# Performance work log

Measured on AMD Instinct MI355X. Metric: run time of the kernel, lower is better.

## Reference

```python
import jax, jax.numpy as jnp
import numpy as np
from jax import lax

B, T, D_IN, D_CB, K_CB, H_MID = 32, 512, 1024, 256, 8192, 512

def setup_inputs() -> dict:
    key = jax.random.key(0)
    ks = jax.random.split(key, 12)
    s = 0.02
    return {
        "x": jax.random.normal(ks[0], (B, T, D_IN), jnp.float32),
        "w1": jax.random.normal(ks[1], (H_MID, D_IN), jnp.float32) * s,
        "b1": jnp.zeros((H_MID,), jnp.float32),
        "w2": jax.random.normal(ks[2], (D_CB, H_MID), jnp.float32) * s,
        "b2": jnp.zeros((D_CB,), jnp.float32),
        "conv_w": jax.random.normal(ks[3], (D_CB, D_CB, 3), jnp.float32) * s,
        "conv_b": jnp.zeros((D_CB,), jnp.float32),
        "codebook": jax.random.uniform(ks[4], (K_CB, D_CB), jnp.float32, -1.0 / K_CB, 1.0 / K_CB),
        "gru_wih": jax.random.normal(ks[5], (3 * D_CB, D_CB), jnp.float32) * s,
        "gru_whh": jax.random.normal(ks[6], (3 * D_CB, D_CB), jnp.float32) * s,
        "gru_bih": jnp.zeros((3 * D_CB,), jnp.float32),
        "gru_bhh": jnp.zeros((3 * D_CB,), jnp.float32),
    }

def _forward(x, w1, b1, w2, b2, conv_w, conv_b, codebook, gru_wih, gru_whh, gru_bih, gru_bhh):
    # feature_processor (dropout is identity at eval): [B,T,D_IN] -> [B,T,D_CB]
    h = jax.nn.relu(jnp.einsum('btd,hd->bth', x, w1) + b1)
    h = jax.nn.relu(jnp.einsum('bth,ch->btc', h, w2) + b2)
    # temporal conv1d, kernel 3, pad 1 (T > 1 here)
    f = jnp.transpose(h, (0, 2, 1))  # NCT
    f = lax.conv_general_dilated(f, conv_w, (1,), 'SAME', dimension_numbers=('NCH', 'OIH', 'NCH'))
    f = f + conv_b[None, :, None]
    features = jnp.transpose(f, (0, 2, 1))  # [B,T,D_CB]
    # quantize: squared-Euclidean nearest codebook entry (same argmin as cdist)
    flat = features.reshape(-1, features.shape[-1])  # [B*T, D_CB]
    d2 = (jnp.sum(flat * flat, axis=1, keepdims=True)
          - 2.0 * (flat @ codebook.T)
          + jnp.sum(codebook * codebook, axis=1))  # [B*T, K]
    idx = jnp.argmin(d2, axis=-1)
    quantized = codebook[idx].reshape(features.shape)  # [B,T,D_CB]
    token_indices = idx.reshape(features.shape[0], features.shape[1])
    commitment_loss = jnp.mean((features - lax.stop_gradient(quantized)) ** 2)
    codebook_loss = jnp.mean((quantized - lax.stop_gradient(features)) ** 2)
    # context predictor: 1-layer GRU over quantized[:, :-1]
    q_in = quantized[:, :-1]  # [B,T-1,D_CB]
    xproj = jnp.einsum('btd,hd->bth', q_in, gru_wih) + gru_bih  # [B,T-1,3H]
    Hd = quantized.shape[-1]
    def step(hprev, xt):
        gh = hprev @ gru_whh.T + gru_bhh  # [B,3H]
        xr, xz, xn = xt[:, :Hd], xt[:, Hd:2 * Hd], xt[:, 2 * Hd:]
        hr, hz, hn = gh[:, :Hd], gh[:, Hd:2 * Hd], gh[:, 2 * Hd:]
        r = jax.nn.sigmoid(xr + hr)
        z = jax.nn.sigmoid(xz + hz)
        n = jnp.tanh(xn + r * hn)
        hnew = (1.0 - z) * n + z * hprev
        return hnew, hnew
    h0 = jnp.zeros((q_in.shape[0], Hd), q_in.dtype)
    _, hs = lax.scan(step, h0, jnp.transpose(xproj, (1, 0, 2)))
    context = jnp.transpose(hs, (1, 0, 2))  # [B,T-1,D_CB]
    context_loss = jnp.mean((context - features[:, 1:]) ** 2)
    vq_loss = commitment_loss + 0.25 * codebook_loss + 0.1 * context_loss
    return token_indices, quantized, commitment_loss, codebook_loss, context_loss, vq_loss

def reference(x, w1, b1, w2, b2, conv_w, conv_b, codebook, gru_wih, gru_whh, gru_bih, gru_bhh):
    return _forward(x, w1, b1, w2, b2, conv_w, conv_b, codebook, gru_wih, gru_whh, gru_bih, gru_bhh)
```

## Files before the change

kernel.cpp:

```cpp
#include <hip/hip_runtime.h>
#include <math.h>

#define NB 32
#define NT 512
#define NDIN 1024
#define NDCB 256
#define NKCB 8192
#define NHMID 512
#define NROWS (NB*NT)

typedef _Float16 half2_t __attribute__((ext_vector_type(2)));
typedef _Float16 f16x8 __attribute__((ext_vector_type(8)));
typedef __attribute__((ext_vector_type(8))) short bf16x8;
typedef __attribute__((ext_vector_type(8))) unsigned short u16x8;
typedef __attribute__((ext_vector_type(4))) float f32x4;

__device__ __forceinline__ unsigned short f2bf(float x) {
    unsigned int u = __float_as_uint(x);
    return (unsigned short)((u + 0x7fffu + ((u >> 16) & 1u)) >> 16);
}

#if __has_builtin(__builtin_amdgcn_fdot2)
__device__ __forceinline__ float dot2f(half2_t a, half2_t b, float c) {
    return __builtin_amdgcn_fdot2(a, b, c, false);
}
#else
__device__ __forceinline__ float dot2f(half2_t a, half2_t b, float c) {
    return fmaf((float)a[0], (float)b[0], fmaf((float)a[1], (float)b[1], c));
}
#endif

template<bool RELU>
__global__ __launch_bounds__(256) void gemm_nt_f64_kernel(
    const float* __restrict__ A, const float* __restrict__ Bm,
    const float* __restrict__ bias, float* __restrict__ C,
    int M, int N, int K)
{
    __shared__ double a_s[16*64];
    __shared__ double b_s[16*64];
    const int tid = threadIdx.x;
    const int bn0 = blockIdx.x * 64;
    const int bm0 = blockIdx.y * 64;
    const int lr = tid >> 2;
    const int kq = (tid & 3) << 2;
    const int tx = tid & 15, ty = tid >> 4;
    double acc[4][4] = {};
    const float* Ap = A + (size_t)(bm0 + lr) * K + kq;
    const float* Bp = Bm + (size_t)(bn0 + lr) * K + kq;
    for (int kt = 0; kt < K; kt += 16) {
        float4 a = *(const float4*)(Ap + kt);
        float4 b = *(const float4*)(Bp + kt);
        __syncthreads();
        a_s[(kq+0)*64+lr] = (double)a.x; a_s[(kq+1)*64+lr] = (double)a.y;
        a_s[(kq+2)*64+lr] = (double)a.z; a_s[(kq+3)*64+lr] = (double)a.w;
        b_s[(kq+0)*64+lr] = (double)b.x; b_s[(kq+1)*64+lr] = (double)b.y;
        b_s[(kq+2)*64+lr] = (double)b.z; b_s[(kq+3)*64+lr] = (double)b.w;
        __syncthreads();
        #pragma unroll
        for (int kk = 0; kk < 16; kk++) {
            double aa[4], bb[4];
            #pragma unroll
            for (int u = 0; u < 4; u++) { aa[u] = a_s[kk*64 + ty*4 + u]; bb[u] = b_s[kk*64 + tx*4 + u]; }
            #pragma unroll
            for (int i = 0; i < 4; i++)
                #pragma unroll
                for (int j = 0; j < 4; j++)
                    acc[i][j] = fma(aa[i], bb[j], acc[i][j]);
        }
    }
    const float4 b4 = *(const float4*)&bias[bn0 + tx*4];
    const double bc[4] = {(double)b4.x, (double)b4.y, (double)b4.z, (double)b4.w};
    #pragma unroll
    for (int i = 0; i < 4; i++) {
        float o[4];
        #pragma unroll
        for (int j = 0; j < 4; j++) {
            double v = acc[i][j] + bc[j];
            if (RELU) v = fmax(v, 0.0);
            o[j] = (float)v;
        }
        *(float4*)&C[(size_t)(bm0 + ty*4 + i)*N + bn0 + tx*4] =
            make_float4(o[0], o[1], o[2], o[3]);
    }
}

__global__ __launch_bounds__(256) void conv3_f64_kernel(
    const float* __restrict__ H2, const float* __restrict__ W3,
    const float* __restrict__ bias, float* __restrict__ F)
{
    __shared__ double a_s[16*68];
    __shared__ double b_s[3][16*64];
    const int tid = threadIdx.x;
    const int bn0 = blockIdx.x * 64;
    const int bm0 = blockIdx.y * 64;
    const int lr = tid >> 2;
    const int kq = (tid & 3) << 2;
    const int tx = tid & 15, ty = tid >> 4;
    const int tmod = bm0 & (NT-1);
    const bool has_top = (tmod != 0);
    const bool has_bot = (tmod + 64 < NT);
    double acc[4][4] = {};
    for (int kt = 0; kt < NDCB; kt += 16) {
        float4 a = make_float4(0.f,0.f,0.f,0.f);
        if (lr >= 1 || has_top)
            a = *(const float4*)&H2[(size_t)(bm0 - 1 + lr)*NDCB + kt + kq];
        float4 e = make_float4(0.f,0.f,0.f,0.f);
        int l2 = 0, kq2 = 0;
        if (tid < 8) {
            l2 = 64 + (tid >> 2); kq2 = (tid & 3) << 2;
            if (l2 == 64 || has_bot)
                e = *(const float4*)&H2[(size_t)(bm0 - 1 + l2)*NDCB + kt + kq2];
        }
        float4 w[3];
        #pragma unroll
        for (int s = 0; s < 3; s++)
            w[s] = *(const float4*)&W3[(size_t)s*65536 + (size_t)(bn0 + lr)*NDCB + kt + kq];
        __syncthreads();
        a_s[(kq+0)*68+lr]=(double)a.x; a_s[(kq+1)*68+lr]=(double)a.y;
        a_s[(kq+2)*68+lr]=(double)a.z; a_s[(kq+3)*68+lr]=(double)a.w;
        if (tid < 8) {
            a_s[(kq2+0)*68+l2]=(double)e.x; a_s[(kq2+1)*68+l2]=(double)e.y;
            a_s[(kq2+2)*68+l2]=(double)e.z; a_s[(kq2+3)*68+l2]=(double)e.w;
        }
        #pragma unroll
        for (int s = 0; s < 3; s++) {
            b_s[s][(kq+0)*64+lr]=(double)w[s].x; b_s[s][(kq+1)*64+lr]=(double)w[s].y;
            b_s[s][(kq+2)*64+lr]=(double)w[s].z; b_s[s][(kq+3)*64+lr]=(double)w[s].w;
        }
        __syncthreads();
        #pragma unroll
        for (int kk = 0; kk < 16; kk++) {
            double aa[6];
            #pragma unroll
            for (int u = 0; u < 6; u++) aa[u] = a_s[kk*68 + ty*4 + u];
            #pragma unroll
            for (int s = 0; s < 3; s++) {
                double bb[4];
                #pragma unroll
                for (int u = 0; u < 4; u++) bb[u] = b_s[s][kk*64 + tx*4 + u];
                #pragma unroll
                for (int i = 0; i < 4; i++)
                    #pragma unroll
                    for (int j = 0; j < 4; j++)
                        acc[i][j] = fma(aa[i+s], bb[j], acc[i][j]);
            }
        }
    }
    const float4 b4 = *(const float4*)&bias[bn0 + tx*4];
    const double bc[4] = {(double)b4.x, (double)b4.y, (double)b4.z, (double)b4.w};
    #pragma unroll
    for (int i = 0; i < 4; i++) {
        const size_t base = (size_t)(bm0 + ty*4 + i)*NDCB + bn0 + tx*4;
        *(float4*)&F[base] = make_float4((float)(acc[i][0]+bc[0]), (float)(acc[i][1]+bc[1]),
                                         (float)(acc[i][2]+bc[2]), (float)(acc[i][3]+bc[3]));
    }
}

__global__ __launch_bounds__(512) void vq_kernel(
    const float* __restrict__ F, const float* __restrict__ CB,
    const unsigned short* __restrict__ CBH,
    const float* __restrict__ cnorm, float* __restrict__ idx_out,
    float* __restrict__ qout, float* __restrict__ msd_acc)
{
    __shared__ unsigned short a_bf[64*256];
    __shared__ unsigned short b_bf[128*256];
    __shared__ float cn_s[128];
    __shared__ float red_v[64*64];
    __shared__ int   red_i[64*64];
    __shared__ int   bests[64];
    __shared__ int   cand[64][12];
    __shared__ int   ccnt[64];
    const int tid = threadIdx.x;
    const int m0 = blockIdx.x * 64;

    #pragma unroll
    for (int u = 0; u < 4; u++) {
        int e = tid + u*512;
        int row = e >> 5, c = e & 31;
        const float* src = &F[(size_t)(m0+row)*NDCB + c*8];
        float4 f0 = *(const float4*)src;
        float4 f1 = *(const float4*)(src+4);
        u16x8 p;
        p[0]=f2bf(f0.x); p[1]=f2bf(f0.y); p[2]=f2bf(f0.z); p[3]=f2bf(f0.w);
        p[4]=f2bf(f1.x); p[5]=f2bf(f1.y); p[6]=f2bf(f1.z); p[7]=f2bf(f1.w);
        *(u16x8*)((char*)a_bf + row*512 + ((c*16) ^ ((row&7)<<4))) = p;
    }

    const int w = tid >> 6, lane = tid & 63;
    const int l15 = lane & 15, kg = lane >> 4;
    const int rbase = (w & 3) << 4, cbase = (w >> 2) << 6;
    const char* aP = (const char*)a_bf + (size_t)(rbase + l15)*512;
    const char* bP = (const char*)b_bf + (size_t)(cbase + l15)*512;
    const int swz = (lane & 7) << 4;

    float mv1[4], mv2[4]; int mi1[4], mi2[4];
    #pragma unroll
    for (int i = 0; i < 4; i++) { mv1[i]=3.0e38f; mv2[i]=3.0e38f; mi1[i]=0x7fffffff; mi2[i]=0x7fffffff; }

    for (int n0 = 0; n0 < NKCB; n0 += 128) {
        __syncthreads();
        #pragma unroll
        for (int u = 0; u < 8; u++) {
            int e = tid + u*512;
            int row = e >> 5, c = e & 31;
            u16x8 v = *(const u16x8*)&CBH[(size_t)(n0+row)*NDCB + c*8];
            *(u16x8*)((char*)b_bf + row*512 + ((c*16) ^ ((row&7)<<4))) = v;
        }
        if (tid < 128) cn_s[tid] = cnorm[n0 + tid];
        __syncthreads();
        f32x4 acc[4] = {{0.f,0.f,0.f,0.f},{0.f,0.f,0.f,0.f},{0.f,0.f,0.f,0.f},{0.f,0.f,0.f,0.f}};
        #pragma unroll
        for (int kt = 0; kt < 8; kt++) {
            const int ko = (kt*64 + kg*16) ^ swz;
            bf16x8 av = *(const bf16x8*)(aP + ko);
            #pragma unroll
            for (int f = 0; f < 4; f++) {
                bf16x8 bv = *(const bf16x8*)(bP + f*8192 + ko);
                acc[f] = __builtin_amdgcn_mfma_f32_16x16x32_bf16(av, bv, acc[f], 0, 0, 0);
            }
        }
        #pragma unroll
        for (int f = 0; f < 4; f++) {
            const int col = n0 + cbase + f*16 + l15;
            const float cnv = cn_s[cbase + f*16 + l15];
            #pragma unroll
            for (int i = 0; i < 4; i++) {
                float s = fmaf(-2.0f, acc[f][i], cnv);
                if (s < mv1[i]) { mv2[i]=mv1[i]; mi2[i]=mi1[i]; mv1[i]=s; mi1[i]=col; }
                else if (s < mv2[i]) { mv2[i]=s; mi2[i]=col; }
            }
        }
    }
    #pragma unroll
    for (int i = 0; i < 4; i++) {
        const int row = rbase + kg*4 + i;
        const int eb  = (w>>2)*32 + l15*2;
        red_v[row*64 + eb]   = mv1[i]; red_i[row*64 + eb]   = mi1[i];
        red_v[row*64 + eb+1] = mv2[i]; red_i[row*64 + eb+1] = mi2[i];
    }
    __syncthreads();
    if (tid < 64) {
        float bv = 3.0e38f; int bi = 0x7fffffff;
        for (int e = 0; e < 64; e++) {
            float v = red_v[tid*64 + e]; int ii = red_i[tid*64 + e];
            if (v < bv || (v == bv && ii < bi)) { bv = v; bi = ii; }
        }
        int cnt = 0;
        for (int e = 0; e < 64; e++) {
            if (red_v[tid*64 + e] < bv + 1.0e-5f) {
                if (cnt < 12) cand[tid][cnt] = red_i[tid*64 + e];
                cnt++;
            }
        }
        bests[tid] = bi;
        ccnt[tid] = (cnt > 12) ? 12 : cnt;
    }
    __syncthreads();
    {
        const int wid = tid >> 6, lane2 = tid & 63;
        for (int r = wid; r < 64; r += 8) {
            const int nc = ccnt[r];
            if (nc < 2) continue;
            double sf = 0.0;
            #pragma unroll
            for (int u = 0; u < 4; u++) {
                double fv = (double)F[(size_t)(m0+r)*NDCB + lane2*4 + u];
                sf = fma(fv, fv, sf);
            }
            #pragma unroll
            for (int off = 32; off > 0; off >>= 1) sf += __shfl_down(sf, off);
            const float sf32 = (float)sf;
            float bd2 = 0.0f; int bidx = 0x7fffffff;
            for (int c = 0; c < nc; c++) {
                const int k = cand[r][c];
                double g = 0.0;
                #pragma unroll
                for (int u = 0; u < 4; u++) {
                    double cv = (double)CB[(size_t)k*NDCB + lane2*4 + u];
                    double fv = (double)F[(size_t)(m0+r)*NDCB + lane2*4 + u];
                    g = fma(cv, fv, g);
                }
                #pragma unroll
                for (int off = 32; off > 0; off >>= 1) g += __shfl_down(g, off);
                if (lane2 == 0) {
                    const float G32 = (float)g;
                    const float t  = sf32 - 2.0f*G32;
                    const float d2 = t + cnorm[k];
                    if (c == 0 || d2 < bd2 || (d2 == bd2 && k < bidx)) { bd2 = d2; bidx = k; }
                }
            }
            if (lane2 == 0) bests[r] = bidx;
        }
    }
    __syncthreads();
    if (tid < 64) idx_out[m0 + tid] = (float)bests[tid];
    float lsum = 0.0f;
    #pragma unroll
    for (int s = 0; s < 8; s++) {
        int e = tid + s*512;
        int row = e >> 6, kqe = (e & 63) << 2;
        float4 q = *(const float4*)&CB[(size_t)bests[row]*NDCB + kqe];
        float4 f = *(const float4*)&F[(size_t)(m0+row)*NDCB + kqe];
        float dx=f.x-q.x, dy=f.y-q.y, dz=f.z-q.z, dw=f.w-q.w;
        lsum += dx*dx + dy*dy + dz*dz + dw*dw;
        *(float4*)&qout[(size_t)(m0+row)*NDCB + kqe] = q;
    }
    red_v[tid] = lsum;
    __syncthreads();
    for (int off = 256; off > 0; off >>= 1) {
        if (tid < off) red_v[tid] += red_v[tid + off];
        __syncthreads();
    }
    if (tid == 0) atomicAdd(msd_acc, red_v[0]);
}

__global__ __launch_bounds__(512) void xproj_mfma_kernel(
    const float* __restrict__ Q, const unsigned short* __restrict__ WIHH,
    const float* __restrict__ bias, float* __restrict__ C)
{
    __shared__ unsigned short a_h[64*256];
    __shared__ unsigned short b_h[128*256];
    const int tid = threadIdx.x;
    const int m0 = blockIdx.x * 64;

    #pragma unroll
    for (int u = 0; u < 4; u++) {
        int e = tid + u*512;
        int row = e >> 5, c = e & 31;
        const float* src = &Q[(size_t)(m0+row)*NDCB + c*8];
        float4 f0 = *(const float4*)src;
        float4 f1 = *(const float4*)(src+4);
        f16x8 p;
        p[0]=(_Float16)(f0.x*8192.0f); p[1]=(_Float16)(f0.y*8192.0f);
        p[2]=(_Float16)(f0.z*8192.0f); p[3]=(_Float16)(f0.w*8192.0f);
        p[4]=(_Float16)(f1.x*8192.0f); p[5]=(_Float16)(f1.y*8192.0f);
        p[6]=(_Float16)(f1.z*8192.0f); p[7]=(_Float16)(f1.w*8192.0f);
        *(f16x8*)((char*)a_h + row*512 + ((c*16) ^ ((row&7)<<4))) = p;
    }

    const int w = tid >> 6, lane = tid & 63;
    const int l15 = lane & 15, kg = lane >> 4;
    const int rbase = (w & 3) << 4, cbase = (w >> 2) << 6;
    const char* aP = (const char*)a_h + (size_t)(rbase + l15)*512;
    const char* bP = (const char*)b_h + (size_t)(cbase + l15)*512;
    const int swz = (lane & 7) << 4;

    for (int n0 = 0; n0 < 768; n0 += 128) {
        __syncthreads();
        #pragma unroll
        for (int u = 0; u < 8; u++) {
            int e = tid + u*512;
            int row = e >> 5, c = e & 31;
            u16x8 v = *(const u16x8*)&WIHH[(size_t)(n0+row)*NDCB + c*8];
            *(u16x8*)((char*)b_h + row*512 + ((c*16) ^ ((row&7)<<4))) = v;
        }
        __syncthreads();
        f32x4 acc[4] = {{0.f,0.f,0.f,0.f},{0.f,0.f,0.f,0.f},{0.f,0.f,0.f,0.f},{0.f,0.f,0.f,0.f}};
        #pragma unroll
        for (int kt = 0; kt < 8; kt++) {
            const int ko = (kt*64 + kg*16) ^ swz;
            f16x8 av = *(const f16x8*)(aP + ko);
            #pragma unroll
            for (int f = 0; f < 4; f++) {
                f16x8 bv = *(const f16x8*)(bP + f*8192 + ko);
                acc[f] = __builtin_amdgcn_mfma_f32_16x16x32_f16(av, bv, acc[f], 0, 0, 0);
            }
        }
        #pragma unroll
        for (int f = 0; f < 4; f++) {
            const int col = n0 + cbase + f*16 + l15;
            const float bv = bias[col];
            #pragma unroll
            for (int i = 0; i < 4; i++) {
                const int row = m0 + rbase + kg*4 + i;
                C[(size_t)row*768 + col] = fmaf(acc[f][i], 1.0f/8192.0f, bv);
            }
        }
    }
}

__device__ __forceinline__ void gru_body_1024(
    const float* __restrict__ XP, const float* __restrict__ WHH,
    const float* __restrict__ bhh, const float* __restrict__ F,
    float* __restrict__ ctx_acc)
{
    __shared__ float part[3][4][256];
    __shared__ uint4 hpk[2][32];
    __shared__ float red[256];
    const int tid = threadIdx.x;
    const int b = blockIdx.x;
    const int j = tid & 255;
    const int q = tid >> 8;
    half2_t wr[32], wz[32], wn[32];
    {
        const float* rp = WHH + (size_t)j*256 + q*64;
        #pragma unroll
        for (int k = 0; k < 16; k++) {
            float4 vr = *(const float4*)(rp + 4*k);
            float4 vz = *(const float4*)(rp + 65536 + 4*k);
            float4 vn = *(const float4*)(rp + 131072 + 4*k);
            wr[2*k+0] = (half2_t){(_Float16)vr.x, (_Float16)vr.y};
            wr[2*k+1] = (half2_t){(_Float16)vr.z, (_Float16)vr.w};
            wz[2*k+0] = (half2_t){(_Float16)vz.x, (_Float16)vz.y};
            wz[2*k+1] = (half2_t){(_Float16)vz.z, (_Float16)vz.w};
            wn[2*k+0] = (half2_t){(_Float16)vn.x, (_Float16)vn.y};
            wn[2*k+1] = (half2_t){(_Float16)vn.z, (_Float16)vn.w};
        }
    }
    if (tid < 64) hpk[tid >> 5][tid & 31] = make_uint4(0u, 0u, 0u, 0u);
    const float bb0 = bhh[j], bb1 = bhh[256+j], bb2 = bhh[512+j];
    const float* xpb = XP + (size_t)b*NT*768;
    const float* fb  = F  + (size_t)b*NT*NDCB;
    float hprev = 0.0f, lsum = 0.0f;
    __syncthreads();
    int cur = 0;
    for (int t = 0; t < NT-1; t++) {
        float xr = 0.f, xz = 0.f, xn = 0.f, fv = 0.f;
        if (tid < 256) {
            const float* xp = xpb + (size_t)t*768;
            xr = xp[j]; xz = xp[256+j]; xn = xp[512+j];
            fv = fb[(size_t)(t+1)*NDCB + j];
        }
        float a0=0.f, c0=0.f, a1=0.f, c1=0.f, a2=0.f, c2=0.f;
        #pragma unroll
        for (int kk = 0; kk < 8; kk++) {
            uint4 hp = hpk[cur][q*8 + kk];
            half2_t h0 = __builtin_bit_cast(half2_t, hp.x);
            half2_t h1 = __builtin_bit_cast(half2_t, hp.y);
            half2_t h2 = __builtin_bit_cast(half2_t, hp.z);
            half2_t h3 = __builtin_bit_cast(half2_t, hp.w);
            a0 = dot2f(wr[4*kk+0], h0, a0); c0 = dot2f(wr[4*kk+1], h1, c0);
            a1 = dot2f(wz[4*kk+0], h0, a1); c1 = dot2f(wz[4*kk+1], h1, c1);
            a2 = dot2f(wn[4*kk+0], h0, a2); c2 = dot2f(wn[4*kk+1], h1, c2);
            a0 = dot2f(wr[4*kk+2], h2, a0); c0 = dot2f(wr[4*kk+3], h3, c0);
            a1 = dot2f(wz[4*kk+2], h2, a1); c1 = dot2f(wz[4*kk+3], h3, c1);
            a2 = dot2f(wn[4*kk+2], h2, a2); c2 = dot2f(wn[4*kk+3], h3, c2);
        }
        part[0][q][j] = a0 + c0; part[1][q][j] = a1 + c1; part[2][q][j] = a2 + c2;
        __syncthreads();
        if (tid < 256) {
            float ghr = part[0][0][j] + part[0][1][j] + part[0][2][j] + part[0][3][j] + bb0;
            float ghz = part[1][0][j] + part[1][1][j] + part[1][2][j] + part[1][3][j] + bb1;
            float ghn = part[2][0][j] + part[2][1][j] + part[2][2][j] + part[2][3][j] + bb2;
            float r = 1.0f/(1.0f + __expf(-(xr + ghr)));
            float z = 1.0f/(1.0f + __expf(-(xz + ghz)));
            float v = fmaf(r, ghn, xn);
            v = fminf(fmaxf(v, -12.0f), 12.0f);
            float ev = __expf(-2.0f*v);
            float n = (1.0f - ev)/(1.0f + ev);
            float hnew = (1.0f - z)*n + z*hprev;
            float d = hnew - fv;
            lsum = fmaf(d, d, lsum);
            float nb = __shfl_down(hnew, 1);
            if (!(j & 1)) {
                half2_t p; p[0] = (_Float16)hnew; p[1] = (_Float16)nb;
                ((unsigned int*)&hpk[cur ^ 1][0])[j >> 1] = __builtin_bit_cast(unsigned int, p);
            }
            hprev = hnew;
        }
        __syncthreads();
        cur ^= 1;
    }
    if (tid < 256) red[j] = lsum;
    __syncthreads();
    for (int off = 128; off > 0; off >>= 1) {
        if (tid < off) red[tid] += red[tid + off];
        __syncthreads();
    }
    if (tid == 0) atomicAdd(ctx_acc, red[0]);
}

__global__ __launch_bounds__(1024, 1)
void gru_w1(const float* __restrict__ XP, const float* __restrict__ WHH,
            const float* __restrict__ bhh, const float* __restrict__ F,
            float* __restrict__ ctx_acc)
{ gru_body_1024(XP, WHH, bhh, F, ctx_acc); }

__global__ __launch_bounds__(1024, 4)
void gru_w2(const float* __restrict__ XP, const float* __restrict__ WHH,
            const float* __restrict__ bhh, const float* __restrict__ F,
            float* __restrict__ ctx_acc)
{ gru_body_1024(XP, WHH, bhh, F, ctx_acc); }

__global__ __attribute__((amdgpu_flat_work_group_size(1024, 1024), amdgpu_waves_per_eu(4, 4)))
void gru_w3(const float* __restrict__ XP, const float* __restrict__ WHH,
            const float* __restrict__ bhh, const float* __restrict__ F,
            float* __restrict__ ctx_acc)
{ gru_body_1024(XP, WHH, bhh, F, ctx_acc); }

__global__ __launch_bounds__(512)
void gru_c(const float* __restrict__ XP, const float* __restrict__ WHH,
           const float* __restrict__ bhh, const float* __restrict__ F,
           float* __restrict__ ctx_acc)
{
    __shared__ float part[3][2][256];
    __shared__ uint4 hpk[2][32];
    __shared__ float red[256];
    const int tid = threadIdx.x;
    const int b = blockIdx.x;
    const int j = tid & 255;
    const int q = tid >> 8;
    half2_t wr[64], wz[64], wn[64];
    {
        const float* rp = WHH + (size_t)j*256 + q*128;
        #pragma unroll
        for (int k = 0; k < 32; k++) {
            float4 vr = *(const float4*)(rp + 4*k);
            float4 vz = *(const float4*)(rp + 65536 + 4*k);
            float4 vn = *(const float4*)(rp + 131072 + 4*k);
            wr[2*k+0] = (half2_t){(_Float16)vr.x, (_Float16)vr.y};
            wr[2*k+1] = (half2_t){(_Float16)vr.z, (_Float16)vr.w};
            wz[2*k+0] = (half2_t){(_Float16)vz.x, (_Float16)vz.y};
            wz[2*k+1] = (half2_t){(_Float16)vz.z, (_Float16)vz.w};
            wn[2*k+0] = (half2_t){(_Float16)vn.x, (_Float16)vn.y};
            wn[2*k+1] = (half2_t){(_Float16)vn.z, (_Float16)vn.w};
        }
    }
    if (tid < 64) hpk[tid >> 5][tid & 31] = make_uint4(0u, 0u, 0u, 0u);
    const float bb0 = bhh[j], bb1 = bhh[256+j], bb2 = bhh[512+j];
    const float* xpb = XP + (size_t)b*NT*768;
    const float* fb  = F  + (size_t)b*NT*NDCB;
    float hprev = 0.0f, lsum = 0.0f;
    __syncthreads();
    int cur = 0;
    for (int t = 0; t < NT-1; t++) {
        float xr = 0.f, xz = 0.f, xn = 0.f, fv = 0.f;
        if (tid < 256) {
            const float* xp = xpb + (size_t)t*768;
            xr = xp[j]; xz = xp[256+j]; xn = xp[512+j];
            fv = fb[(size_t)(t+1)*NDCB + j];
        }
        float a0=0.f, c0=0.f, a1=0.f, c1=0.f, a2=0.f, c2=0.f;
        #pragma unroll
        for (int kk = 0; kk < 16; kk++) {
            uint4 hp = hpk[cur][q*16 + kk];
            half2_t h0 = __builtin_bit_cast(half2_t, hp.x);
            half2_t h1 = __builtin_bit_cast(half2_t, hp.y);
            half2_t h2 = __builtin_bit_cast(half2_t, hp.z);
            half2_t h3 = __builtin_bit_cast(half2_t, hp.w);
            a0 = dot2f(wr[4*kk+0], h0, a0); c0 = dot2f(wr[4*kk+1], h1, c0);
            a1 = dot2f(wz[4*kk+0], h0, a1); c1 = dot2f(wz[4*kk+1], h1, c1);
            a2 = dot2f(wn[4*kk+0], h0, a2); c2 = dot2f(wn[4*kk+1], h1, c2);
            a0 = dot2f(wr[4*kk+2], h2, a0); c0 = dot2f(wr[4*kk+3], h3, c0);
            a1 = dot2f(wz[4*kk+2], h2, a1); c1 = dot2f(wz[4*kk+3], h3, c1);
            a2 = dot2f(wn[4*kk+2], h2, a2); c2 = dot2f(wn[4*kk+3], h3, c2);
        }
        part[0][q][j] = a0 + c0; part[1][q][j] = a1 + c1; part[2][q][j] = a2 + c2;
        __syncthreads();
        if (tid < 256) {
            float ghr = part[0][0][j] + part[0][1][j] + bb0;
            float ghz = part[1][0][j] + part[1][1][j] + bb1;
            float ghn = part[2][0][j] + part[2][1][j] + bb2;
            float r = 1.0f/(1.0f + __expf(-(xr + ghr)));
            float z = 1.0f/(1.0f + __expf(-(xz + ghz)));
            float v = fmaf(r, ghn, xn);
            v = fminf(fmaxf(v, -12.0f), 12.0f);
            float ev = __expf(-2.0f*v);
            float n = (1.0f - ev)/(1.0f + ev);
            float hnew = (1.0f - z)*n + z*hprev;
            float d = hnew - fv;
            lsum = fmaf(d, d, lsum);
            float nb = __shfl_down(hnew, 1);
            if (!(j & 1)) {
                half2_t p; p[0] = (_Float16)hnew; p[1] = (_Float16)nb;
                ((unsigned int*)&hpk[cur ^ 1][0])[j >> 1] = __builtin_bit_cast(unsigned int, p);
            }
            hprev = hnew;
        }
        __syncthreads();
        cur ^= 1;
    }
    if (tid < 256) red[j] = lsum;
    __syncthreads();
    for (int off = 128; off > 0; off >>= 1) {
        if (tid < off) red[tid] += red[tid + off];
        __syncthreads();
    }
    if (tid == 0) atomicAdd(ctx_acc, red[0]);
}

__global__ __launch_bounds__(256) void prep_kernel(
    const float* __restrict__ conv_w, float* __restrict__ w3,
    const float* __restrict__ wih, unsigned short* __restrict__ wihh,
    float* __restrict__ accv)
{
    int e = blockIdx.x*256 + threadIdx.x;
    if (e == 0) { accv[0] = 0.0f; accv[1] = 0.0f; }
    {
        int k = e >> 16;
        int r = e & 65535;
        int c = r >> 8, i = r & 255;
        w3[e] = conv_w[(size_t)c*768 + i*3 + k];
    }
    {
        _Float16 h = (_Float16)wih[e];
        wihh[e] = __builtin_bit_cast(unsigned short, h);
    }
}

__global__ __launch_bounds__(256) void cb2bf_kernel(
    const float* __restrict__ cb, unsigned short* __restrict__ cbh)
{
    int e = (blockIdx.x*256 + threadIdx.x) * 4;
    float4 v = *(const float4*)&cb[e];
    unsigned short p0 = f2bf(v.x), p1 = f2bf(v.y), p2 = f2bf(v.z), p3 = f2bf(v.w);
    unsigned long long pk = (unsigned long long)p0 | ((unsigned long long)p1 << 16)
                          | ((unsigned long long)p2 << 32) | ((unsigned long long)p3 << 48);
    *(unsigned long long*)&cbh[e] = pk;
}

__global__ __launch_bounds__(64) void cnorm_kernel(
    const float* __restrict__ CB, float* __restrict__ cn)
{
    const int k = blockIdx.x;
    const int lane = threadIdx.x;
    float4 v = *(const float4*)&CB[(size_t)k*NDCB + lane*4];
    double s = (double)v.x*(double)v.x + (double)v.y*(double)v.y
             + (double)v.z*(double)v.z + (double)v.w*(double)v.w;
    #pragma unroll
    for (int off = 32; off > 0; off >>= 1) s += __shfl_down(s, off);
    if (lane == 0) cn[k] = (float)s;
}

__global__ void finalize_kernel(const float* __restrict__ acc, float* __restrict__ out)
{
    if (threadIdx.x == 0) {
        float msd = acc[0] * (1.0f/4194304.0f);
        float ctx = acc[1] * (1.0f/4184064.0f);
        out[0] = msd;
        out[1] = msd;
        out[2] = ctx;
        out[3] = 1.25f*msd + 0.1f*ctx;
    }
}

extern "C" void kernel_launch(void* const* d_in, const int* in_sizes, int n_in,
                              void* d_out, int out_size, void* d_ws, size_t ws_size,
                              hipStream_t stream) {
    const float* x      = (const float*)d_in[0];
    const float* w1     = (const float*)d_in[1];
    const float* b1     = (const float*)d_in[2];
    const float* w2     = (const float*)d_in[3];
    const float* b2     = (const float*)d_in[4];
    const float* conv_w = (const float*)d_in[5];
    const float* conv_b = (const float*)d_in[6];
    const float* cb     = (const float*)d_in[7];
    const float* wih    = (const float*)d_in[8];
    const float* whh    = (const float*)d_in[9];
    const float* bih    = (const float*)d_in[10];
    const float* bhh    = (const float*)d_in[11];
    float* out = (float*)d_out;

    char* ws = (char*)d_ws;
    float*  feat   = (float*)(ws + 0);
    float*  h1     = (float*)(ws + 16777216);
    float*  xproj  = (float*)(ws + 16777216);
    float*  h2     = (float*)(ws + 50331648);
    unsigned short* cbh = (unsigned short*)(ws + 50331648);
    float*  cn     = (float*)(ws + 67108864);
    float*  w3     = (float*)(ws + 67141632);
    unsigned short* wihh = (unsigned short*)(ws + 67928064);
    float*  accv   = (float*)(ws + 68714496);

    float* idx_out = out;
    float* qout    = out + 16384;
    float* louts   = out + 16384 + 4194304;

    static int gsel = -1;
    if (gsel < 0) {
        const void* cands[3] = {
            reinterpret_cast<const void*>(gru_w1),
            reinterpret_cast<const void*>(gru_w2),
            reinterpret_cast<const void*>(gru_w3) };
        gsel = 3;
        for (int pass = 0; pass < 2 && gsel == 3; ++pass) {
            size_t lim = (pass == 0) ? 0 : 64;
            for (int i = 0; i < 3 && gsel == 3; ++i) {
                hipFuncAttributes fa;
                if (hipFuncGetAttributes(&fa, cands[i]) == hipSuccess
                    && fa.localSizeBytes <= lim && fa.numRegs >= 116) gsel = i;
            }
        }
    }

    prep_kernel<<<768, 256, 0, stream>>>(conv_w, w3, wih, wihh, accv);
    cnorm_kernel<<<NKCB, 64, 0, stream>>>(cb, cn);
    gemm_nt_f64_kernel<true ><<<dim3(NHMID/64, NROWS/64), 256, 0, stream>>>(x,  w1, b1, h1, NROWS, NHMID, NDIN);
    gemm_nt_f64_kernel<true ><<<dim3(NDCB/64,  NROWS/64), 256, 0, stream>>>(h1, w2, b2, h2, NROWS, NDCB, NHMID);
    conv3_f64_kernel<<<dim3(NDCB/64, NROWS/64), 256, 0, stream>>>(h2, w3, conv_b, feat);
    cb2bf_kernel<<<2048, 256, 0, stream>>>(cb, cbh);
    vq_kernel<<<NROWS/64, 512, 0, stream>>>(feat, cb, cbh, cn, idx_out, qout, accv);
    xproj_mfma_kernel<<<NROWS/64, 512, 0, stream>>>(qout, wihh, bih, xproj);
    if (gsel == 0)      gru_w1<<<NB, 1024, 0, stream>>>(xproj, whh, bhh, feat, accv + 1);
    else if (gsel == 1) gru_w2<<<NB, 1024, 0, stream>>>(xproj, whh, bhh, feat, accv + 1);
    else if (gsel == 2) gru_w3<<<NB, 1024, 0, stream>>>(xproj, whh, bhh, feat, accv + 1);
    else                gru_c<<<NB, 512, 0, stream>>>(xproj, whh, bhh, feat, accv + 1);
    finalize_kernel<<<1, 64, 0, stream>>>(accv, louts);
}
```

Measured before the change: 1.762 ms.

## Add gate-split 768-thread GRU variant and spill-aware kernel selection

Adds a GRU recurrence kernel where each of three 256-thread groups computes one full gate row (r, z or n) over all 256 hidden inputs. This removes the cross-thread partial-sum reduction through shared memory at every time step. The 1024-thread body now keeps the bias in shared memory and uses strided pointer increments to save registers. Kernel choice becomes a scoring heuristic that weighs a hardcoded base cost against reported scratch spill bytes. The risk is spills, since the new variant holds 128 half2 weight registers per thread.

```diff
diff --git a/kernel.cpp b/kernel.cpp
--- a/kernel.cpp
+++ b/kernel.cpp
@@ -18,6 +18,10 @@
 __device__ __forceinline__ unsigned short f2bf(float x) {
     unsigned int u = __float_as_uint(x);
     return (unsigned short)((u + 0x7fffu + ((u >> 16) & 1u)) >> 16);
+}
+
+__device__ __forceinline__ half2_t h2of(unsigned int u) {
+    return __builtin_bit_cast(half2_t, u);
 }
 
 #if __has_builtin(__builtin_amdgcn_fdot2)
@@ -379,6 +383,7 @@
     }
 }
 
+
 __device__ __forceinline__ void gru_body_1024(
     const float* __restrict__ XP, const float* __restrict__ WHH,
     const float* __restrict__ bhh, const float* __restrict__ F,
@@ -387,6 +392,7 @@
     __shared__ float part[3][4][256];
     __shared__ uint4 hpk[2][32];
     __shared__ float red[256];
+    __shared__ float bbs[3][256];
     const int tid = threadIdx.x;
     const int b = blockIdx.x;
     const int j = tid & 255;
@@ -408,27 +414,24 @@
         }
     }
     if (tid < 64) hpk[tid >> 5][tid & 31] = make_uint4(0u, 0u, 0u, 0u);
-    const float bb0 = bhh[j], bb1 = bhh[256+j], bb2 = bhh[512+j];
-    const float* xpb = XP + (size_t)b*NT*768;
-    const float* fb  = F  + (size_t)b*NT*NDCB;
+    if (tid < 256) { bbs[0][j] = bhh[j]; bbs[1][j] = bhh[256+j]; bbs[2][j] = bhh[512+j]; }
+    const float* xq = XP + (size_t)b*NT*768 + j;
+    const float* fq = F  + (size_t)b*NT*NDCB + NDCB + j;
     float hprev = 0.0f, lsum = 0.0f;
     __syncthreads();
     int cur = 0;
     for (int t = 0; t < NT-1; t++) {
         float xr = 0.f, xz = 0.f, xn = 0.f, fv = 0.f;
         if (tid < 256) {
-            const float* xp = xpb + (size_t)t*768;
-            xr = xp[j]; xz = xp[256+j]; xn = xp[512+j];
-            fv = fb[(size_t)(t+1)*NDCB + j];
+            xr = xq[0]; xz = xq[256]; xn = xq[512];
+            fv = *fq;
+            xq += 768; fq += 256;
         }
         float a0=0.f, c0=0.f, a1=0.f, c1=0.f, a2=0.f, c2=0.f;
         #pragma unroll
         for (int kk = 0; kk < 8; kk++) {
             uint4 hp = hpk[cur][q*8 + kk];
-            half2_t h0 = __builtin_bit_cast(half2_t, hp.x);
-            half2_t h1 = __builtin_bit_cast(half2_t, hp.y);
-            half2_t h2 = __builtin_bit_cast(half2_t, hp.z);
-            half2_t h3 = __builtin_bit_cast(half2_t, hp.w);
+            half2_t h0 = h2of(hp.x), h1 = h2of(hp.y), h2 = h2of(hp.z), h3 = h2of(hp.w);
             a0 = dot2f(wr[4*kk+0], h0, a0); c0 = dot2f(wr[4*kk+1], h1, c0);
             a1 = dot2f(wz[4*kk+0], h0, a1); c1 = dot2f(wz[4*kk+1], h1, c1);
             a2 = dot2f(wn[4*kk+0], h0, a2); c2 = dot2f(wn[4*kk+1], h1, c2);
@@ -439,9 +442,9 @@
         part[0][q][j] = a0 + c0; part[1][q][j] = a1 + c1; part[2][q][j] = a2 + c2;
         __syncthreads();
         if (tid < 256) {
-            float ghr = part[0][0][j] + part[0][1][j] + part[0][2][j] + part[0][3][j] + bb0;
-            float ghz = part[1][0][j] + part[1][1][j] + part[1][2][j] + part[1][3][j] + bb1;
-            float ghn = part[2][0][j] + part[2][1][j] + part[2][2][j] + part[2][3][j] + bb2;
+            float ghr = part[0][0][j] + part[0][1][j] + part[0][2][j] + part[0][3][j] + bbs[0][j];
+            float ghz = part[1][0][j] + part[1][1][j] + part[1][2][j] + part[1][3][j] + bbs[1][j];
+            float ghn = part[2][0][j] + part[2][1][j] + part[2][2][j] + part[2][3][j] + bbs[2][j];
             float r = 1.0f/(1.0f + __expf(-(xr + ghr)));
             float z = 1.0f/(1.0f + __expf(-(xz + ghz)));
             float v = fmaf(r, ghn, xn);
@@ -476,17 +479,100 @@
             float* __restrict__ ctx_acc)
 { gru_body_1024(XP, WHH, bhh, F, ctx_acc); }
 
-__global__ __launch_bounds__(1024, 4)
-void gru_w2(const float* __restrict__ XP, const float* __restrict__ WHH,
-            const float* __restrict__ bhh, const float* __restrict__ F,
-            float* __restrict__ ctx_acc)
-{ gru_body_1024(XP, WHH, bhh, F, ctx_acc); }
-
 __global__ __attribute__((amdgpu_flat_work_group_size(1024, 1024), amdgpu_waves_per_eu(4, 4)))
 void gru_w3(const float* __restrict__ XP, const float* __restrict__ WHH,
             const float* __restrict__ bhh, const float* __restrict__ F,
             float* __restrict__ ctx_acc)
 { gru_body_1024(XP, WHH, bhh, F, ctx_acc); }
+
+__device__ __forceinline__ void gru_body_768(
+    const float* __restrict__ XP, const float* __restrict__ WHH,
+    const float* __restrict__ bhh, const float* __restrict__ F,
+    float* __restrict__ ctx_acc)
+{
+    __shared__ float sg[3][256];
+    __shared__ float xs[256];
+    __shared__ uint4 hpk[2][32];
+    __shared__ float red[256];
+    const int tid = threadIdx.x;
+    const int b = blockIdx.x;
+    const int g = tid >> 8;
+    const int j = tid & 255;
+    half2_t wg[128];
+    {
+        const float* rp = WHH + ((size_t)g*256 + j)*256;
+        #pragma unroll
+        for (int k = 0; k < 32; k++) {
+            float4 v = *(const float4*)(rp + 4*k);
+            wg[2*k+0] = (half2_t){(_Float16)v.x, (_Float16)v.y};
+            wg[2*k+1] = (half2_t){(_Float16)v.z, (_Float16)v.w};
+        }
+    }
+    if (tid < 64) hpk[tid >> 5][tid & 31] = make_uint4(0u, 0u, 0u, 0u);
+    const float bbg = bhh[g*256 + j];
+    const float* xq = XP + (size_t)b*NT*768 + g*256 + j;
+    const float* fq = F  + (size_t)b*NT*NDCB + NDCB + j;
+    float hprev = 0.0f, lsum = 0.0f;
+    __syncthreads();
+    int cur = 0;
+    for (int t = 0; t < NT-1; t++) {
+        float xg = *xq; xq += 768;
+        float fv = 0.f;
+        if (g == 0) { fv = *fq; fq += 256; }
+        float a0 = 0.f, a1 = 0.f;
+        #pragma unroll
+        for (int kk = 0; kk < 32; kk += 2) {
+            uint4 hp0 = hpk[cur][kk];
+            uint4 hp1 = hpk[cur][kk+1];
+            a0 = dot2f(wg[4*kk+0], h2of(hp0.x), a0); a1 = dot2f(wg[4*kk+1], h2of(hp0.y), a1);
+            a0 = dot2f(wg[4*kk+2], h2of(hp0.z), a0); a1 = dot2f(wg[4*kk+3], h2of(hp0.w), a1);
+            a0 = dot2f(wg[4*kk+4], h2of(hp1.x), a0); a1 = dot2f(wg[4*kk+5], h2of(hp1.y), a1);
+            a0 = dot2f(wg[4*kk+6], h2of(hp1.z), a0); a1 = dot2f(wg[4*kk+7], h2of(hp1.w), a1);
+        }
+        float gh = a0 + a1 + bbg;
+        if (g == 2) { sg[2][j] = gh; xs[j] = xg; }
+        else        { sg[g][j] = gh + xg; }
+        __syncthreads();
+        if (tid < 256) {
+            float r = 1.0f/(1.0f + __expf(-sg[0][j]));
+            float z = 1.0f/(1.0f + __expf(-sg[1][j]));
+            float v = fmaf(r, sg[2][j], xs[j]);
+            v = fminf(fmaxf(v, -12.0f), 12.0f);
+            float ev = __expf(-2.0f*v);
+            float n = (1.0f - ev)/(1.0f + ev);
+            float hnew = (1.0f - z)*n + z*hprev;
+            float d = hnew - fv;
+            lsum = fmaf(d, d, lsum);
+            float nb = __shfl_down(hnew, 1);
+            if (!(j & 1)) {
+                half2_t p; p[0] = (_Float16)hnew; p[1] = (_Float16)nb;
+                ((unsigned int*)&hpk[cur ^ 1][0])[j >> 1] = __builtin_bit_cast(unsigned int, p);
+            }
+            hprev = hnew;
+        }
+        __syncthreads();
+        cur ^= 1;
+    }
+    if (tid < 256) red[j] = lsum;
+    __syncthreads();
+    for (int off = 128; off > 0; off >>= 1) {
+        if (tid < off) red[tid] += red[tid + off];
+        __syncthreads();
+    }
+    if (tid == 0) atomicAdd(ctx_acc, red[0]);
+}
+
+__global__ __attribute__((amdgpu_flat_work_group_size(768, 768), amdgpu_waves_per_eu(3, 3)))
+void gru_v1(const float* __restrict__ XP, const float* __restrict__ WHH,
+            const float* __restrict__ bhh, const float* __restrict__ F,
+            float* __restrict__ ctx_acc)
+{ gru_body_768(XP, WHH, bhh, F, ctx_acc); }
+
+__global__ __launch_bounds__(768)
+void gru_v2(const float* __restrict__ XP, const float* __restrict__ WHH,
+            const float* __restrict__ bhh, const float* __restrict__ F,
+            float* __restrict__ ctx_acc)
+{ gru_body_768(XP, WHH, bhh, F, ctx_acc); }
 
 __global__ __launch_bounds__(512)
 void gru_c(const float* __restrict__ XP, const float* __restrict__ WHH,
@@ -534,10 +620,7 @@
         #pragma unroll
         for (int kk = 0; kk < 16; kk++) {
             uint4 hp = hpk[cur][q*16 + kk];
-            half2_t h0 = __builtin_bit_cast(half2_t, hp.x);
-            half2_t h1 = __builtin_bit_cast(half2_t, hp.y);
-            half2_t h2 = __builtin_bit_cast(half2_t, hp.z);
-            half2_t h3 = __builtin_bit_cast(half2_t, hp.w);
+            half2_t h0 = h2of(hp.x), h1 = h2of(hp.y), h2 = h2of(hp.z), h3 = h2of(hp.w);
             a0 = dot2f(wr[4*kk+0], h0, a0); c0 = dot2f(wr[4*kk+1], h1, c0);
             a1 = dot2f(wz[4*kk+0], h0, a1); c1 = dot2f(wz[4*kk+1], h1, c1);
             a2 = dot2f(wn[4*kk+0], h0, a2); c2 = dot2f(wn[4*kk+1], h1, c2);
@@ -668,18 +751,21 @@
 
     static int gsel = -1;
     if (gsel < 0) {
-        const void* cands[3] = {
-            reinterpret_cast<const void*>(gru_w1),
-            reinterpret_cast<const void*>(gru_w2),
-            reinterpret_cast<const void*>(gru_w3) };
-        gsel = 3;
-        for (int pass = 0; pass < 2 && gsel == 3; ++pass) {
-            size_t lim = (pass == 0) ? 0 : 64;
-            for (int i = 0; i < 3 && gsel == 3; ++i) {
-                hipFuncAttributes fa;
-                if (hipFuncGetAttributes(&fa, cands[i]) == hipSuccess
-                    && fa.localSizeBytes <= lim && fa.numRegs >= 116) gsel = i;
-            }
+        struct Cand { const void* f; long thr; long base; };
+        const Cand cands[5] = {
+            { reinterpret_cast<const void*>(gru_w1), 1024,  800 },
+            { reinterpret_cast<const void*>(gru_w3), 1024,  800 },
+            { reinterpret_cast<const void*>(gru_v1),  768, 1550 },
+            { reinterpret_cast<const void*>(gru_v2),  768, 1550 },
+            { reinterpret_cast<const void*>(gru_c),   512, 1650 },
+        };
+        long best = 0x7fffffffffffL;
+        gsel = 4;
+        for (int i = 0; i < 5; i++) {
+            hipFuncAttributes fa;
+            if (hipFuncGetAttributes(&fa, cands[i].f) != hipSuccess) continue;
+            long score = cands[i].base + (long)fa.localSizeBytes * cands[i].thr * 5 / 1024;
+            if (score < best) { best = score; gsel = i; }
         }
     }
 
@@ -692,8 +778,9 @@
     vq_kernel<<<NROWS/64, 512, 0, stream>>>(feat, cb, cbh, cn, idx_out, qout, accv);
     xproj_mfma_kernel<<<NROWS/64, 512, 0, stream>>>(qout, wihh, bih, xproj);
     if (gsel == 0)      gru_w1<<<NB, 1024, 0, stream>>>(xproj, whh, bhh, feat, accv + 1);
-    else if (gsel == 1) gru_w2<<<NB, 1024, 0, stream>>>(xproj, whh, bhh, feat, accv + 1);
-    else if (gsel == 2) gru_w3<<<NB, 1024, 0, stream>>>(xproj, whh, bhh, feat, accv + 1);
-    else                gru_c<<<NB, 512, 0, stream>>>(xproj, whh, bhh, feat, accv + 1);
+    else if (gsel == 1) gru_w3<<<NB, 1024, 0, stream>>>(xproj, whh, bhh, feat, accv + 1);
+    else if (gsel == 2) gru_v1<<<NB,  768, 0, stream>>>(xproj, whh, bhh, feat, accv + 1);
+    else if (gsel == 3) gru_v2<<<NB,  768, 0, stream>>>(xproj, whh, bhh, feat, accv + 1);
+    else                gru_c<<<NB,  512, 0, stream>>>(xproj, whh, bhh, feat, accv + 1);
     finalize_kernel<<<1, 64, 0, stream>>>(accv, louts);
 }
```

Result: no change. 1.791 ms (+1.7%).
